# Optimization experiments

Hardware: AMD Instinct MI355X
Metric: run time of the kernel (lower is better)

Reference implementation:

```python
import jax, jax.numpy as jnp
import numpy as np

B, S, D = 2, 2048, 2048
HQ, HKV = 32, 8
DH = D // HQ  # 64
NUM_REP = HQ // HKV  # 4


def setup_inputs() -> dict:
    key = jax.random.key(0)
    k1, k2, k3, k4, k5 = jax.random.split(key, 5)
    scale = 0.02
    return {
        "x": jax.random.normal(k1, (B, S, D), dtype=jnp.float32),
        "Wq": jax.random.normal(k2, (D, HQ * DH), dtype=jnp.float32) * scale,
        "Wk": jax.random.normal(k3, (D, HKV * DH), dtype=jnp.float32) * scale,
        "Wv": jax.random.normal(k4, (D, HKV * DH), dtype=jnp.float32) * scale,
        "Wo": jax.random.normal(k5, (HQ * DH, D), dtype=jnp.float32) * scale,
    }


def reference(x, Wq, Wk, Wv, Wo):
    b, s, _ = x.shape
    # projections
    xq = (x @ Wq).reshape(b, s, HQ, DH)    # [B,S,HQ,DH]
    xk = (x @ Wk).reshape(b, s, HKV, DH)   # [B,S,HKV,DH]
    xv = (x @ Wv).reshape(b, s, HKV, DH)
    # repeat kv heads to match query heads (GQA expand)
    keys = jnp.repeat(xk, NUM_REP, axis=2)    # [B,S,HQ,DH]
    values = jnp.repeat(xv, NUM_REP, axis=2)
    # scores: [B,HQ,S,S], fp32 softmax (no causal mask in original)
    scores = jnp.einsum("bqhd,bkhd->bhqk", xq, keys) / jnp.sqrt(jnp.float32(DH))
    probs = jax.nn.softmax(scores.astype(jnp.float32), axis=-1).astype(xq.dtype)
    context = jnp.einsum("bhqk,bkhd->bqhd", probs, values)  # [B,S,HQ,DH]
    context = context.reshape(b, s, HQ * DH)
    return context @ Wo
```

## Files before the change

kernel.cpp:

```cpp
#include <hip/hip_runtime.h>
#include <cstdint>
#include <cstddef>
#include <cmath>

typedef __bf16 bf16x8 __attribute__((ext_vector_type(8)));
typedef float  f32x4  __attribute__((ext_vector_type(4)));
typedef unsigned short us4 __attribute__((ext_vector_type(4)));

__device__ __forceinline__ unsigned short f2bf(float f) {
    union { float f; unsigned int u; } v; v.f = f;
    unsigned int u = v.u;
    u += 0x7fffu + ((u >> 16) & 1u);
    return (unsigned short)(u >> 16);
}

__device__ __forceinline__ unsigned int fbits(float f) {
    union { float f; unsigned int u; } v; v.f = f; return v.u;
}

__device__ __forceinline__ unsigned int pk_bf16_trunc(float a, float b) {
    return __builtin_amdgcn_perm(fbits(b), fbits(a), 0x07060302u);
}

__device__ __forceinline__ void gld_lds16(const void* g, void* l) {
    __builtin_amdgcn_global_load_lds((__attribute__((address_space(1))) void*)g,
                                     (__attribute__((address_space(3))) void*)l,
                                     16, 0, 0);
}

#define BB   2
#define SS   2048
#define DD   2048
#define HQ   32
#define HKV  8
#define DH   64
#define MM   (BB * SS)
#define NQKV 3072

#define QSCALE 0.18033688011112042f

__global__ __launch_bounds__(256) void prep(const float* __restrict__ x,
                                            const float* __restrict__ Wq,
                                            const float* __restrict__ Wk,
                                            const float* __restrict__ Wv,
                                            const float* __restrict__ Wo,
                                            unsigned short* __restrict__ xb,
                                            unsigned short* __restrict__ WqkvT,
                                            unsigned short* __restrict__ WoT) {
    const int bid = blockIdx.x;
    if (bid < 8192) {
        const int i = (bid * 256 + threadIdx.x) * 4;
        const float4 f = *(const float4*)(x + i);
        us4 o;
        o[0] = f2bf(f.x); o[1] = f2bf(f.y); o[2] = f2bf(f.z); o[3] = f2bf(f.w);
        *(us4*)(xb + i) = o;
        return;
    }
    const float* src; unsigned short* dst; int C, bx, by; float scl = 1.0f;
    int r = bid - 8192;
    if (r < 4096) {
        src = Wq; dst = WqkvT; C = 2048; bx = r & 63; by = r >> 6; scl = QSCALE;
    } else if (r < 8192) {
        r -= 4096; src = Wo; dst = WoT; C = 2048; bx = r & 63; by = r >> 6;
    } else if (r < 9216) {
        r -= 8192; src = Wk; dst = WqkvT + (size_t)2048 * 2048; C = 512; bx = r & 15; by = r >> 4;
    } else {
        r -= 9216; src = Wv; dst = WqkvT + (size_t)2560 * 2048; C = 512; bx = r & 15; by = r >> 4;
    }
    const int R = 2048;
    __shared__ __attribute__((aligned(16))) float tile[32][33];
    const int c0 = bx * 32, r0 = by * 32;
    const int tx = threadIdx.x & 31, ty = threadIdx.x >> 5;
    #pragma unroll
    for (int dy = 0; dy < 32; dy += 8)
        tile[ty + dy][tx] = src[(size_t)(r0 + ty + dy) * C + c0 + tx];
    __syncthreads();
    #pragma unroll
    for (int dy = 0; dy < 32; dy += 8)
        dst[(size_t)(c0 + ty + dy) * R + r0 + tx] = f2bf(tile[tx][ty + dy] * scl);
}

__global__ __launch_bounds__(256) void transpose_v(const unsigned short* __restrict__ qkv,
                                                   unsigned short* __restrict__ vt) {
    __shared__ __attribute__((aligned(16))) unsigned short tile[32][33];
    const int s0 = blockIdx.x * 32, d0 = blockIdx.y * 32;
    const int bh = blockIdx.z;
    const int b = bh >> 3, kvh = bh & 7;
    const int tx = threadIdx.x & 31, ty = threadIdx.x >> 5;
    #pragma unroll
    for (int dy = 0; dy < 32; dy += 8)
        tile[ty + dy][tx] =
            qkv[(size_t)(b * SS + s0 + ty + dy) * NQKV + 2560 + kvh * DH + d0 + tx];
    __syncthreads();
    #pragma unroll
    for (int dy = 0; dy < 32; dy += 8)
        vt[(size_t)((b * HKV + kvh) * DH + d0 + ty + dy) * SS + s0 + tx] =
            tile[tx][ty + dy];
}

__global__ __launch_bounds__(512, 2) void gemm192(const unsigned short* __restrict__ A,
                                                  const unsigned short* __restrict__ Bt,
                                                  unsigned short* __restrict__ Cout,
                                                  int M, int N, int K) {
    __shared__ __attribute__((aligned(16))) unsigned short As[2][256 * 64];
    __shared__ __attribute__((aligned(16))) unsigned short Bs[2][192 * 64];
    const int lid = blockIdx.x;
    const int bm = ((lid & 7) << 1) | ((lid >> 3) & 1);
    const int bn = lid >> 4;
    const int tid = threadIdx.x;
    const int wv = tid >> 6, lane = tid & 63;
    const int wm = (wv >> 2) * 128;
    const int wn = (wv & 3) * 48;
    const int g = lane >> 4, l15 = lane & 15;
    const int sr = lane >> 3;
    const int sc8 = ((lane & 7) ^ (sr & 7)) * 8;
    const int r7 = l15 & 7;

    f32x4 acc[8][3] = {};
    const unsigned short* spA[4];
    const unsigned short* spB[3];
    #pragma unroll
    for (int j = 0; j < 4; ++j)
        spA[j] = A + (size_t)(bm * 256 + (wv * 4 + j) * 8 + sr) * K + sc8;
    #pragma unroll
    for (int j = 0; j < 3; ++j)
        spB[j] = Bt + (size_t)(bn * 192 + wv * 24 + j * 8 + sr) * K + sc8;

    #define GSTAGE(BUF)                                                       \
        do {                                                                  \
            _Pragma("unroll")                                                 \
            for (int j = 0; j < 4; ++j) {                                     \
                gld_lds16(spA[j], &As[BUF][(wv * 4 + j) * 512]);              \
                spA[j] += 64;                                                 \
            }                                                                 \
            _Pragma("unroll")                                                 \
            for (int j = 0; j < 3; ++j) {                                     \
                gld_lds16(spB[j], &Bs[BUF][(wv * 3 + j) * 512]);              \
                spB[j] += 64;                                                 \
            }                                                                 \
        } while (0)

    #define GCOMPUTE(BUF)                                                     \
        do {                                                                  \
            const unsigned short* as = As[BUF];                               \
            const unsigned short* bs = Bs[BUF];                               \
            bf16x8 bfr[3][2];                                                 \
            _Pragma("unroll")                                                 \
            for (int n = 0; n < 3; ++n)                                       \
                _Pragma("unroll")                                             \
                for (int ks = 0; ks < 2; ++ks)                                \
                    bfr[n][ks] = *(const bf16x8*)&bs[(wn + n * 16 + l15) * 64 \
                                                 + ((ks * 4 + g) ^ r7) * 8];  \
            _Pragma("unroll")                                                 \
            for (int q = 0; q < 4; ++q) {                                     \
                bf16x8 af[2][2];                                              \
                _Pragma("unroll")                                             \
                for (int mi = 0; mi < 2; ++mi)                                \
                    _Pragma("unroll")                                         \
                    for (int ks = 0; ks < 2; ++ks)                            \
                        af[mi][ks] = *(const bf16x8*)&as[                     \
                            (wm + (q * 2 + mi) * 16 + l15) * 64               \
                            + ((ks * 4 + g) ^ r7) * 8];                       \
                _Pragma("unroll")                                             \
                for (int ks = 0; ks < 2; ++ks)                                \
                    _Pragma("unroll")                                         \
                    for (int mi = 0; mi < 2; ++mi)                            \
                        _Pragma("unroll")                                     \
                        for (int n = 0; n < 3; ++n)                           \
                            acc[q * 2 + mi][n] =                              \
                                __builtin_amdgcn_mfma_f32_16x16x32_bf16(      \
                                    af[mi][ks], bfr[n][ks],                   \
                                    acc[q * 2 + mi][n], 0, 0, 0);             \
            }                                                                 \
        } while (0)

    GSTAGE(0);
    GSTAGE(1);
    asm volatile("s_waitcnt vmcnt(7)" ::: "memory");
    __builtin_amdgcn_s_barrier();

    #pragma unroll 1
    for (int t2 = 0; t2 < 16; ++t2) {
        GCOMPUTE(0);
        __builtin_amdgcn_s_barrier();
        if (t2 < 15) {
            GSTAGE(0);
            asm volatile("s_waitcnt vmcnt(7)" ::: "memory");
        } else {
            asm volatile("s_waitcnt vmcnt(0)" ::: "memory");
        }
        __builtin_amdgcn_s_barrier();
        GCOMPUTE(1);
        if (t2 == 15) break;
        __builtin_amdgcn_s_barrier();
        GSTAGE(1);
        asm volatile("s_waitcnt vmcnt(7)" ::: "memory");
        __builtin_amdgcn_s_barrier();
    }

    #pragma unroll
    for (int i = 0; i < 8; ++i) {
        #pragma unroll
        for (int n = 0; n < 3; ++n) {
            const int col = bn * 192 + wn + n * 16 + l15;
            #pragma unroll
            for (int r = 0; r < 4; ++r) {
                const int row = bm * 256 + wm + i * 16 + g * 4 + r;
                Cout[(size_t)row * N + col] = f2bf(acc[i][n][r]);
            }
        }
    }
    #undef GSTAGE
    #undef GCOMPUTE
}

template <int OUT_BF16>
__global__ __launch_bounds__(256) void gemm_bt(const unsigned short* __restrict__ A,
                                               const unsigned short* __restrict__ Bt,
                                               void* __restrict__ Cout,
                                               int M, int N, int K) {
    __shared__ __attribute__((aligned(16))) unsigned short As[128 * 64];
    __shared__ __attribute__((aligned(16))) unsigned short Bs[128 * 64];
    const int bm = blockIdx.x, bn = blockIdx.y;
    const int tid = threadIdx.x;
    const int wave = tid >> 6, lane = tid & 63;
    const int wm = (wave >> 1) * 64, wn = (wave & 1) * 64;
    const int g = lane >> 4, l15 = lane & 15;
    const int sr = lane >> 3;
    const int sc8 = ((lane & 7) ^ (sr & 7)) * 8;
    const int r7 = l15 & 7;

    f32x4 acc[4][4] = {};
    const unsigned short* aBase = A  + (size_t)(bm * 128) * K;
    const unsigned short* bBase = Bt + (size_t)(bn * 128) * K;

    for (int kt = 0; kt < K; kt += 64) {
        __syncthreads();
        #pragma unroll
        for (int j = 0; j < 4; ++j) {
            const int i = wave * 4 + j;
            gld_lds16(aBase + (size_t)(i * 8 + sr) * K + kt + sc8, &As[i * 512]);
            gld_lds16(bBase + (size_t)(i * 8 + sr) * K + kt + sc8, &Bs[i * 512]);
        }
        __syncthreads();
        #pragma unroll
        for (int ks = 0; ks < 2; ++ks) {
            bf16x8 af[4], bfr[4];
            #pragma unroll
            for (int t = 0; t < 4; ++t) {
                af[t]  = *(const bf16x8*)&As[(wm + t * 16 + l15) * 64 + ((ks * 4 + g) ^ r7) * 8];
                bfr[t] = *(const bf16x8*)&Bs[(wn + t * 16 + l15) * 64 + ((ks * 4 + g) ^ r7) * 8];
            }
            #pragma unroll
            for (int i = 0; i < 4; ++i)
                #pragma unroll
                for (int j = 0; j < 4; ++j)
                    acc[i][j] = __builtin_amdgcn_mfma_f32_16x16x32_bf16(
                        af[i], bfr[j], acc[i][j], 0, 0, 0);
        }
    }
    #pragma unroll
    for (int i = 0; i < 4; ++i) {
        #pragma unroll
        for (int j = 0; j < 4; ++j) {
            const int col = bn * 128 + wn + j * 16 + l15;
            #pragma unroll
            for (int r = 0; r < 4; ++r) {
                const int row = bm * 128 + wm + i * 16 + g * 4 + r;
                const float v = acc[i][j][r];
                if (OUT_BF16)
                    ((unsigned short*)Cout)[(size_t)row * N + col] = f2bf(v);
                else
                    ((float*)Cout)[(size_t)row * N + col] = v;
            }
        }
    }
}

__global__ __launch_bounds__(256, 4) void flash_attn(const unsigned short* __restrict__ qkv,
                                                     const unsigned short* __restrict__ vt,
                                                     unsigned short* __restrict__ ctx) {
    __shared__ __attribute__((aligned(16))) unsigned short Ks[2][64 * 64];
    __shared__ __attribute__((aligned(16))) unsigned short Vs[2][64 * 64];

    const int qt = blockIdx.x, h = blockIdx.y, b = blockIdx.z;
    const int kvh = h >> 2;
    const int tid = threadIdx.x, wave = tid >> 6, lane = tid & 63;
    const int g = lane >> 4, l15 = lane & 15;
    const int sr = lane >> 3;
    const int sc8 = ((lane & 7) ^ (sr & 7)) * 8;
    const int r7 = l15 & 7;
    const int qb = qt * 128 + wave * 32;

    const unsigned short* kbase = qkv + (size_t)(b * SS) * NQKV + 2048 + kvh * DH;
    const unsigned short* vbase = vt + (size_t)((b * HKV + kvh) * DH) * SS;

    bf16x8 qf[2][2];
    #pragma unroll
    for (int n = 0; n < 2; ++n)
        #pragma unroll
        for (int kh = 0; kh < 2; ++kh)
            qf[n][kh] = *(const bf16x8*)(qkv +
                (size_t)(b * SS + qb + n * 16 + l15) * NQKV + h * DH + kh * 32 + g * 8);

    bf16x8 ones;
    #pragma unroll
    for (int i = 0; i < 8; ++i) ones[i] = (__bf16)1.0f;

    const f32x4 z4 = {0.0f, 0.0f, 0.0f, 0.0f};

    const unsigned short* sp[4];
    size_t sadv;
    if (wave < 2) {
        #pragma unroll
        for (int j = 0; j < 4; ++j) {
            const int rho = (wave * 4 + j) * 8 + sr;
            const int key = (rho & 0x23) | ((rho & 0x0C) << 1) | ((rho & 0x10) >> 2);
            sp[j] = kbase + (size_t)key * NQKV + sc8;
        }
        sadv = (size_t)64 * NQKV;
    } else {
        #pragma unroll
        for (int j = 0; j < 4; ++j)
            sp[j] = vbase + (size_t)(((wave - 2) * 4 + j) * 8 + sr) * SS + sc8;
        sadv = 64;
    }

    #define STAGE(buf)                                                        \
        do {                                                                  \
            if (wave < 2) {                                                   \
                _Pragma("unroll")                                             \
                for (int j = 0; j < 4; ++j)                                   \
                    gld_lds16(sp[j], &Ks[buf][(wave * 4 + j) * 512]);         \
            } else {                                                          \
                _Pragma("unroll")                                             \
                for (int j = 0; j < 4; ++j)                                   \
                    gld_lds16(sp[j], &Vs[buf][((wave - 2) * 4 + j) * 512]);   \
            }                                                                 \
            _Pragma("unroll")                                                 \
            for (int j = 0; j < 4; ++j) sp[j] += sadv;                        \
        } while (0)

    f32x4 oacc[2][4] = {};
    f32x4 lacc[2] = {};

    #define TILE(BUF)                                                                          \
        do {                                                                                   \
            const unsigned short* ks = Ks[BUF];                                                \
            const unsigned short* vs = Vs[BUF];                                                \
            _Pragma("unroll")                                                                  \
            for (int p = 0; p < 2; ++p) {                                                      \
                uint4 pk4[2];                                                                  \
                _Pragma("unroll")                                                              \
                for (int hh = 0; hh < 2; ++hh) {                                               \
                    const int t = 2 * p + hh;                                                  \
                    bf16x8 kf0 = *(const bf16x8*)&ks[(t * 16 + l15) * 64 + ((g) ^ r7) * 8];    \
                    bf16x8 kf1 = *(const bf16x8*)&ks[(t * 16 + l15) * 64 + ((4 + g) ^ r7) * 8];\
                    _Pragma("unroll")                                                          \
                    for (int n = 0; n < 2; ++n) {                                              \
                        f32x4 c = __builtin_amdgcn_mfma_f32_16x16x32_bf16(                     \
                            kf0, qf[n][0], z4, 0, 0, 0);                                       \
                        c = __builtin_amdgcn_mfma_f32_16x16x32_bf16(                           \
                            kf1, qf[n][1], c, 0, 0, 0);                                        \
                        f32x4 pe;                                                              \
                        pe[0] = __builtin_amdgcn_exp2f(c[0]);                                  \
                        pe[1] = __builtin_amdgcn_exp2f(c[1]);                                  \
                        pe[2] = __builtin_amdgcn_exp2f(c[2]);                                  \
                        pe[3] = __builtin_amdgcn_exp2f(c[3]);                                  \
                        const unsigned int lo = pk_bf16_trunc(pe[0], pe[1]);                   \
                        const unsigned int hi = pk_bf16_trunc(pe[2], pe[3]);                   \
                        if (hh == 0) { pk4[n].x = lo; pk4[n].y = hi; }                         \
                        else         { pk4[n].z = lo; pk4[n].w = hi; }                         \
                    }                                                                          \
                }                                                                              \
                __builtin_amdgcn_s_setprio(1);                                                 \
                _Pragma("unroll")                                                              \
                for (int nt = 0; nt < 4; ++nt) {                                               \
                    bf16x8 vf = *(const bf16x8*)&vs[(nt * 16 + l15) * 64 +                     \
                                                    (((p << 2) + g) ^ r7) * 8];                \
                    _Pragma("unroll")                                                          \
                    for (int m = 0; m < 2; ++m) {                                              \
                        union { uint4 u; bf16x8 v; } pa; pa.u = pk4[m];                        \
                        oacc[m][nt] = __builtin_amdgcn_mfma_f32_16x16x32_bf16(                 \
                            pa.v, vf, oacc[m][nt], 0, 0, 0);                                   \
                        if (nt == 0)                                                           \
                            lacc[m] = __builtin_amdgcn_mfma_f32_16x16x32_bf16(                 \
                                pa.v, ones, lacc[m], 0, 0, 0);                                 \
                    }                                                                          \
                }                                                                              \
                __builtin_amdgcn_s_setprio(0);                                                 \
            }                                                                                  \
        } while (0)

    STAGE(0);

    #pragma unroll 1
    for (int kt2 = 0; kt2 < 16; ++kt2) {
        __syncthreads();
        STAGE(1);
        TILE(0);
        __syncthreads();
        if (kt2 < 15) STAGE(0);
        TILE(1);
    }

    #pragma unroll
    for (int m = 0; m < 2; ++m) {
        #pragma unroll
        for (int r = 0; r < 4; ++r) {
            const float inv = __builtin_amdgcn_rcpf(lacc[m][r]);
            const int token = b * SS + qb + m * 16 + g * 4 + r;
            #pragma unroll
            for (int nt = 0; nt < 4; ++nt)
                ctx[(size_t)token * (HQ * DH) + h * DH + nt * 16 + l15] =
                    f2bf(oacc[m][nt][r] * inv);
        }
    }
    #undef TILE
    #undef STAGE
}

extern "C" void kernel_launch(void* const* d_in, const int* in_sizes, int n_in,
                              void* d_out, int out_size, void* d_ws, size_t ws_size,
                              hipStream_t stream) {
    (void)in_sizes; (void)n_in; (void)out_size; (void)ws_size;
    const float* x  = (const float*)d_in[0];
    const float* Wq = (const float*)d_in[1];
    const float* Wk = (const float*)d_in[2];
    const float* Wv = (const float*)d_in[3];
    const float* Wo = (const float*)d_in[4];
    float* out = (float*)d_out;

    char* ws = (char*)d_ws;
    unsigned short* xb     = (unsigned short*)(ws);
    unsigned short* WqkvT  = (unsigned short*)(ws + 16777216);
    unsigned short* WoT    = (unsigned short*)(ws + 29360128);
    unsigned short* QKV    = (unsigned short*)(ws + 37748736);
    unsigned short* Vt     = (unsigned short*)(ws + 62914560);
    unsigned short* ctx    = (unsigned short*)(ws + 67108864);

    prep<<<18432, 256, 0, stream>>>(x, Wq, Wk, Wv, Wo, xb, WqkvT, WoT);

    gemm192<<<256, 512, 0, stream>>>(xb, WqkvT, QKV, MM, NQKV, DD);

    transpose_v<<<dim3(64, 2, 16), 256, 0, stream>>>(QKV, Vt);

    flash_attn<<<dim3(16, 32, 2), 256, 0, stream>>>(QKV, Vt, ctx);

    gemm_bt<0><<<dim3(32, 16), 256, 0, stream>>>(ctx, WoT, out, MM, DD, DD);
}
```

Baseline: 276.0 us.

## Replace output projection GEMM with double-buffered 256x128 tile kernel

Replaces the simple single-buffered 128x128 output-projection GEMM with a 512-thread kernel that computes 256x128 tiles. It double-buffers the LDS stages and uses explicit vmcnt waits and barriers, so global-to-LDS loads overlap MFMA compute. It also remaps block indices to group M-tiles for better L2 reuse of weights. In exchange it uses more LDS per block and more hand-tuned synchronization, which could introduce hazards if the wait counts are wrong.

Result: slower. 291.3 us (+5.5%).

```diff
diff --git a/kernel.cpp b/kernel.cpp
--- a/kernel.cpp
+++ b/kernel.cpp
@@ -214,67 +214,120 @@
     #undef GCOMPUTE
 }
 
-template <int OUT_BF16>
-__global__ __launch_bounds__(256) void gemm_bt(const unsigned short* __restrict__ A,
-                                               const unsigned short* __restrict__ Bt,
-                                               void* __restrict__ Cout,
-                                               int M, int N, int K) {
-    __shared__ __attribute__((aligned(16))) unsigned short As[128 * 64];
-    __shared__ __attribute__((aligned(16))) unsigned short Bs[128 * 64];
-    const int bm = blockIdx.x, bn = blockIdx.y;
+__global__ __launch_bounds__(512, 2) void gemm128o(const unsigned short* __restrict__ A,
+                                                   const unsigned short* __restrict__ Bt,
+                                                   float* __restrict__ Cout,
+                                                   int M, int N, int K) {
+    __shared__ __attribute__((aligned(16))) unsigned short As[2][256 * 64];
+    __shared__ __attribute__((aligned(16))) unsigned short Bs[2][128 * 64];
+    const int lid = blockIdx.x;
+    const int bm = ((lid & 7) << 1) | ((lid >> 3) & 1);
+    const int bn = lid >> 4;
     const int tid = threadIdx.x;
-    const int wave = tid >> 6, lane = tid & 63;
-    const int wm = (wave >> 1) * 64, wn = (wave & 1) * 64;
+    const int wv = tid >> 6, lane = tid & 63;
+    const int wm = (wv >> 2) * 128;
+    const int wn = (wv & 3) * 32;
     const int g = lane >> 4, l15 = lane & 15;
     const int sr = lane >> 3;
     const int sc8 = ((lane & 7) ^ (sr & 7)) * 8;
     const int r7 = l15 & 7;
 
-    f32x4 acc[4][4] = {};
-    const unsigned short* aBase = A  + (size_t)(bm * 128) * K;
-    const unsigned short* bBase = Bt + (size_t)(bn * 128) * K;
-
-    for (int kt = 0; kt < K; kt += 64) {
-        __syncthreads();
+    f32x4 acc[8][2] = {};
+    const unsigned short* spA[4];
+    const unsigned short* spB[2];
+    #pragma unroll
+    for (int j = 0; j < 4; ++j)
+        spA[j] = A + (size_t)(bm * 256 + (wv * 4 + j) * 8 + sr) * K + sc8;
+    #pragma unroll
+    for (int j = 0; j < 2; ++j)
+        spB[j] = Bt + (size_t)(bn * 128 + wv * 16 + j * 8 + sr) * K + sc8;
+
+    #define OSTAGE(BUF)                                                       \
+        do {                                                                  \
+            _Pragma("unroll")                                                 \
+            for (int j = 0; j < 4; ++j) {                                     \
+                gld_lds16(spA[j], &As[BUF][(wv * 4 + j) * 512]);              \
+                spA[j] += 64;                                                 \
+            }                                                                 \
+            _Pragma("unroll")                                                 \
+            for (int j = 0; j < 2; ++j) {                                     \
+                gld_lds16(spB[j], &Bs[BUF][(wv * 2 + j) * 512]);              \
+                spB[j] += 64;                                                 \
+            }                                                                 \
+        } while (0)
+
+    #define OCOMPUTE(BUF)                                                     \
+        do {                                                                  \
+            const unsigned short* as = As[BUF];                               \
+            const unsigned short* bs = Bs[BUF];                               \
+            bf16x8 bfr[2][2];                                                 \
+            _Pragma("unroll")                                                 \
+            for (int n = 0; n < 2; ++n)                                       \
+                _Pragma("unroll")                                             \
+                for (int ks = 0; ks < 2; ++ks)                                \
+                    bfr[n][ks] = *(const bf16x8*)&bs[(wn + n * 16 + l15) * 64 \
+                                                 + ((ks * 4 + g) ^ r7) * 8];  \
+            _Pragma("unroll")                                                 \
+            for (int q = 0; q < 4; ++q) {                                     \
+                bf16x8 af[2][2];                                              \
+                _Pragma("unroll")                                             \
+                for (int mi = 0; mi < 2; ++mi)                                \
+                    _Pragma("unroll")                                         \
+                    for (int ks = 0; ks < 2; ++ks)                            \
+                        af[mi][ks] = *(const bf16x8*)&as[                     \
+                            (wm + (q * 2 + mi) * 16 + l15) * 64               \
+                            + ((ks * 4 + g) ^ r7) * 8];                       \
+                _Pragma("unroll")                                             \
+                for (int ks = 0; ks < 2; ++ks)                                \
+                    _Pragma("unroll")                                         \
+                    for (int mi = 0; mi < 2; ++mi)                            \
+                        _Pragma("unroll")                                     \
+                        for (int n = 0; n < 2; ++n)                           \
+                            acc[q * 2 + mi][n] =                              \
+                                __builtin_amdgcn_mfma_f32_16x16x32_bf16(      \
+                                    af[mi][ks], bfr[n][ks],                   \
+                                    acc[q * 2 + mi][n], 0, 0, 0);             \
+            }                                                                 \
+        } while (0)
+
+    OSTAGE(0);
+    OSTAGE(1);
+    asm volatile("s_waitcnt vmcnt(6)" ::: "memory");
+    __builtin_amdgcn_s_barrier();
+
+    #pragma unroll 1
+    for (int t2 = 0; t2 < 16; ++t2) {
+        OCOMPUTE(0);
+        __builtin_amdgcn_s_barrier();
+        if (t2 < 15) {
+            OSTAGE(0);
+            asm volatile("s_waitcnt vmcnt(6)" ::: "memory");
+        } else {
+            asm volatile("s_waitcnt vmcnt(0)" ::: "memory");
+        }
+        __builtin_amdgcn_s_barrier();
+        OCOMPUTE(1);
+        if (t2 == 15) break;
+        __builtin_amdgcn_s_barrier();
+        OSTAGE(1);
+        asm volatile("s_waitcnt vmcnt(6)" ::: "memory");
+        __builtin_amdgcn_s_barrier();
+    }
+
+    #pragma unroll
+    for (int i = 0; i < 8; ++i) {
         #pragma unroll
-        for (int j = 0; j < 4; ++j) {
-            const int i = wave * 4 + j;
-            gld_lds16(aBase + (size_t)(i * 8 + sr) * K + kt + sc8, &As[i * 512]);
-            gld_lds16(bBase + (size_t)(i * 8 + sr) * K + kt + sc8, &Bs[i * 512]);
-        }
-        __syncthreads();
-        #pragma unroll
-        for (int ks = 0; ks < 2; ++ks) {
-            bf16x8 af[4], bfr[4];
-            #pragma unroll
-            for (int t = 0; t < 4; ++t) {
-                af[t]  = *(const bf16x8*)&As[(wm + t * 16 + l15) * 64 + ((ks * 4 + g) ^ r7) * 8];
-                bfr[t] = *(const bf16x8*)&Bs[(wn + t * 16 + l15) * 64 + ((ks * 4 + g) ^ r7) * 8];
-            }
-            #pragma unroll
-            for (int i = 0; i < 4; ++i)
-                #pragma unroll
-                for (int j = 0; j < 4; ++j)
-                    acc[i][j] = __builtin_amdgcn_mfma_f32_16x16x32_bf16(
-                        af[i], bfr[j], acc[i][j], 0, 0, 0);
-        }
-    }
-    #pragma unroll
-    for (int i = 0; i < 4; ++i) {
-        #pragma unroll
-        for (int j = 0; j < 4; ++j) {
-            const int col = bn * 128 + wn + j * 16 + l15;
+        for (int n = 0; n < 2; ++n) {
+            const int col = bn * 128 + wn + n * 16 + l15;
             #pragma unroll
             for (int r = 0; r < 4; ++r) {
-                const int row = bm * 128 + wm + i * 16 + g * 4 + r;
-                const float v = acc[i][j][r];
-                if (OUT_BF16)
-                    ((unsigned short*)Cout)[(size_t)row * N + col] = f2bf(v);
-                else
-                    ((float*)Cout)[(size_t)row * N + col] = v;
+                const int row = bm * 256 + wm + i * 16 + g * 4 + r;
+                Cout[(size_t)row * N + col] = acc[i][n][r];
             }
         }
     }
+    #undef OSTAGE
+    #undef OCOMPUTE
 }
 
 __global__ __launch_bounds__(256, 4) void flash_attn(const unsigned short* __restrict__ qkv,
@@ -447,5 +500,5 @@
 
     flash_attn<<<dim3(16, 32, 2), 256, 0, stream>>>(QKV, Vt, ctx);
 
-    gemm_bt<0><<<dim3(32, 16), 256, 0, stream>>>(ctx, WoT, out, MM, DD, DD);
-}
+    gemm128o<<<256, 512, 0, stream>>>(ctx, WoT, out, MM, DD, DD);
+}
```
